# Kernel optimization log

Hardware: AMD Instinct MI355X
Metric: run time of the kernel (lower is better)

## Reference

```python
import jax, jax.numpy as jnp
import numpy as np

N, M = 1024, 32
FN, FE = 64, 32
AGG_N, AGG_E = 128, 64
OUT_N, OUT_E = 64, 32


def _build_indices(n, m):
    nip, eip = [], []
    k = 0
    for i in range(1, n):
        j0 = max(0, i - m)
        nip += list(range(j0, i))
        eip += list(range(k, k + i - j0))
        k += i - j0
    n1 = np.array(nip, np.int32)
    eT = np.array(eip, np.int32)
    n2 = np.concatenate([np.full(min(i, m), i, np.int32) for i in range(1, n)])
    # padded previous-node window indices (0 = zero pad slot)
    prev_nodes = np.zeros(n * m, np.int32)
    k = 0
    for i in range(n):
        t = min(i, m)
        prev_nodes[(i + 1) * m - t:(i + 1) * m] = np.arange(k, k + t) + 1
        k += t
    n_e = k
    norm_node = np.full(n, 1.0 / m, np.float32)
    for i in range(1, m):
        norm_node[i] = 1.0 / i
    prev_edges = np.zeros(n_e * m, np.int32)
    k = 0
    e = 0
    for i in range(n):
        j0 = max(0, i - m)
        for j in range(j0, i):
            if j > j0:
                prev_edges[(e + 1) * m - (j - j0):(e + 1) * m] = np.arange(k, k + j - j0) + 1
            e += 1
        k += i - j0
    norm_edge = np.ones(n_e, np.float32)
    k = 0
    for i in range(1, n):
        t = min(i, m)
        for j in range(t):
            if j > 0:
                norm_edge[k] = 1.0 / j
            k += 1
    return n1, eT, n2, prev_nodes, norm_node, prev_edges, norm_edge, n_e

N1, ET, N2, PREV_N, NORM_N, PREV_E, NORM_E, NE = _build_indices(N, M)
N1 = jnp.asarray(N1); ET = jnp.asarray(ET); N2 = jnp.asarray(N2)
PREV_N = jnp.asarray(PREV_N); PREV_E = jnp.asarray(PREV_E)
NORM_N = jnp.asarray(NORM_N); NORM_E = jnp.asarray(NORM_E)


def setup_inputs() -> dict:
    key = jax.random.key(0)
    ks = jax.random.split(key, 20)
    s = 0.02
    inp = {
        'input_nodes': jax.random.normal(ks[0], (2, N, FN), jnp.float32),
        'input_edges': jax.random.normal(ks[1], (2, NE, FE), jnp.float32),
        # node-branch MLPs (exclude_last=False)
        'Wan1': jax.random.normal(ks[2], (2 * FN + FE, 2 * AGG_N)) * s,
        'ban1': jnp.zeros((2 * AGG_N,)),
        'Wan2': jax.random.normal(ks[3], (2 * AGG_N, AGG_N)) * s,
        'ban2': jnp.zeros((AGG_N,)),
        'Wln1': jax.random.normal(ks[4], (AGG_N + FN, AGG_N + FN)) * s,
        'bln1': jnp.zeros((AGG_N + FN,)),
        'Wln2': jax.random.normal(ks[5], (AGG_N + FN, OUT_N)) * s,
        'bln2': jnp.zeros((OUT_N,)),
        # edge-branch MLPs
        'Wae1': jax.random.normal(ks[6], (FN + FE, 2 * AGG_E)) * s,
        'bae1': jnp.zeros((2 * AGG_E,)),
        'Wae2': jax.random.normal(ks[7], (2 * AGG_E, AGG_E)) * s,
        'bae2': jnp.zeros((AGG_E,)),
        'Wle1': jax.random.normal(ks[8], (AGG_E + FE, AGG_E + FE)) * s,
        'ble1': jnp.zeros((AGG_E + FE,)),
        'Wle2': jax.random.normal(ks[9], (AGG_E + FE, OUT_E)) * s,
        'ble2': jnp.zeros((OUT_E,)),
    }
    return inp


def _mlp2(x, W1, b1, W2, b2):
    return jax.nn.relu(jax.nn.relu(x @ W1 + b1) @ W2 + b2)


def reference(input_nodes, input_edges, Wan1, ban1, Wan2, ban2, Wln1, bln1, Wln2, bln2,
              Wae1, bae1, Wae2, bae2, Wle1, ble1, Wle2, ble2):
    B = input_nodes.shape[0]
    # gather node-edge pairs [B, NE, FN+FE] and node-edge-node triples [B, NE, 2FN+FE]
    pairs = jnp.concatenate([input_nodes[:, N1], input_edges[:, ET]], axis=-1)
    triples = jnp.concatenate([input_nodes[:, N1], input_edges[:, ET], input_nodes[:, N2]], axis=-1)
    # node branch (exclude_last=False -> triples)
    hn = _mlp2(triples, Wan1, ban1, Wan2, ban2)                     # [B, NE, AGG_N]
    hn = jnp.concatenate([jnp.zeros((B, 1, AGG_N), hn.dtype), hn], axis=1)
    pn = hn[:, PREV_N].reshape(B, N, M, AGG_N).sum(axis=2)          # padded window sum
    pn = pn * NORM_N[None, :, None]
    nodes_in = jnp.concatenate([pn, input_nodes], axis=-1)
    out_nodes = _mlp2(nodes_in, Wln1, bln1, Wln2, bln2)             # activation_nodes = relu
    # edge branch (pairs)
    he = _mlp2(pairs, Wae1, bae1, Wae2, bae2)                       # [B, NE, AGG_E]
    he = jnp.concatenate([jnp.zeros((B, 1, AGG_E), he.dtype), he], axis=1)
    pe = he[:, PREV_E].reshape(B, NE, M, AGG_E).sum(axis=2)
    pe = pe * NORM_E[None, :, None]
    edges_in = jnp.concatenate([pe, input_edges], axis=-1)
    out_edges = _mlp2(edges_in, Wle1, ble1, Wle2, ble2)             # activation_edges = relu
    return out_nodes, out_edges
```

## Files before the change

kernel.cpp:

```cpp
#include <hip/hip_runtime.h>
#include <cstdint>

#define NN    1024
#define MM    32
#define NEDGE 32240
#define MROWS 64480
#define PX    168
#define PST   392
#define PLB   104
#define PHE   72

typedef unsigned short ushort_t;

typedef __bf16 bf16x8 __attribute__((ext_vector_type(8)));
typedef float  floatx4 __attribute__((ext_vector_type(4)));

__device__ __forceinline__ float b2f(ushort_t u) {
    union { unsigned int i; float f; } v; v.i = ((unsigned int)u) << 16; return v.f;
}
__device__ __forceinline__ ushort_t f2b(float f) {
    return __builtin_bit_cast(ushort_t, (__bf16)f);
}
__device__ __forceinline__ int edge_base(int i) {
    return (i <= MM) ? ((i * (i - 1)) >> 1) : (496 + (i - MM) * MM);
}

__global__ __launch_bounds__(256) void k_pack(
        const float* an1, const float* an2, const float* ae1, const float* ae2,
        const float* le1, const float* le2, const float* ln1, const float* ln2,
        const float* nodes,
        ushort_t* pan1, ushort_t* pan2, ushort_t* pae1, ushort_t* pae2,
        ushort_t* ple1, ushort_t* ple2, ushort_t* pln1, ushort_t* pln2,
        ushort_t* nodesb) {
    __shared__ float tile[32][33];
    const int bid = blockIdx.x;
    const int tid = threadIdx.x;
    if (bid < 152) {
        const float* s; ushort_t* d; int K, N, t;
        if (bid < 40)       { s = an1; d = pan1; K = 160; N = 256; t = bid;       }
        else if (bid < 72)  { s = an2; d = pan2; K = 256; N = 128; t = bid - 40;  }
        else if (bid < 84)  { s = ae1; d = pae1; K = 96;  N = 128; t = bid - 72;  }
        else if (bid < 92)  { s = ae2; d = pae2; K = 128; N = 64;  t = bid - 84;  }
        else if (bid < 101) { s = le1; d = ple1; K = 96;  N = 96;  t = bid - 92;  }
        else if (bid < 104) { s = le2; d = ple2; K = 96;  N = 32;  t = bid - 101; }
        else if (bid < 140) { s = ln1; d = pln1; K = 192; N = 192; t = bid - 104; }
        else                { s = ln2; d = pln2; K = 192; N = 64;  t = bid - 140; }
        int ntn = N >> 5;
        int tk = t / ntn, tn = t - tk * ntn;
        int k0 = tk * 32, n0 = tn * 32;
        int tx = tid & 31, ty = tid >> 5;
#pragma unroll
        for (int m = 0; m < 4; ++m)
            tile[ty + m * 8][tx] = s[(size_t)(k0 + ty + m * 8) * N + n0 + tx];
        __syncthreads();
#pragma unroll
        for (int m = 0; m < 4; ++m)
            d[(size_t)(n0 + ty + m * 8) * K + k0 + tx] = f2b(tile[tx][ty + m * 8]);
    } else {
        int i4 = (bid - 152) * 256 + tid;
        float4 v = ((const float4*)nodes)[i4];
        uint2 o;
        o.x = (unsigned)f2b(v.x) | ((unsigned)f2b(v.y) << 16);
        o.y = (unsigned)f2b(v.z) | ((unsigned)f2b(v.w) << 16);
        ((uint2*)nodesb)[i4] = o;
    }
}

__global__ __launch_bounds__(512, 4) void k_main(
        const ushort_t* __restrict__ nodesb, const float* __restrict__ edges,
        const ushort_t* __restrict__ pan1, const float* __restrict__ ban1,
        const ushort_t* __restrict__ pan2, const float* __restrict__ ban2,
        const ushort_t* __restrict__ pae1, const float* __restrict__ bae1,
        const ushort_t* __restrict__ pae2, const float* __restrict__ bae2,
        const ushort_t* __restrict__ ple1, const float* __restrict__ ble1,
        const ushort_t* __restrict__ ple2, const float* __restrict__ ble2,
        ushort_t* __restrict__ pn, float* __restrict__ out_edges) {
    __shared__ alignas(16) ushort_t X[32 * PX];
    __shared__ alignas(16) ushort_t H[32 * PST];
    __shared__ alignas(16) ushort_t HE[32 * PHE];
    const int tid = threadIdx.x;
    const int w = tid >> 6, l = tid & 63, lrow = l & 15, lq = l >> 4;
    const int bid = blockIdx.x;
    floatx4 zero = {0.f, 0.f, 0.f, 0.f};

    const int b = bid >> 10, i = bid & 1023;
    const int t = min(i, MM);
    if (i == 0) {
        if (tid < 64) ((unsigned*)(pn + (size_t)bid * 128))[tid] = 0u;
        return;
    }
    const int j0 = i - t;
    const int base = b * NEDGE + edge_base(i);

    bf16x8 B0[5], B1[5], B2[3];
#pragma unroll
    for (int kt = 0; kt < 5; ++kt) {
        B0[kt] = *(const bf16x8*)(pan1 + (size_t)(16 * w + lrow) * 160 + kt * 32 + lq * 8);
        B1[kt] = *(const bf16x8*)(pan1 + (size_t)(16 * (w + 8) + lrow) * 160 + kt * 32 + lq * 8);
    }
#pragma unroll
    for (int kt = 0; kt < 3; ++kt)
        B2[kt] = *(const bf16x8*)(pae1 + (size_t)(16 * w + lrow) * 96 + kt * 32 + lq * 8);
    const float c0 = ban1[16 * w + lrow];
    const float c1 = ban1[16 * (w + 8) + lrow];
    const float c2 = bae1[16 * w + lrow];

#pragma unroll
    for (int k = 0; k < 4; ++k) {
        int rr = w * 4 + k;
        unsigned* xr = (unsigned*)(X + rr * PX);
        const unsigned* nj = (const unsigned*)(nodesb + (size_t)(b * NN + j0 + rr) * 64);
        const unsigned* ni = (const unsigned*)(nodesb + (size_t)(b * NN + i) * 64);
        if (l < 32) { xr[l] = nj[l]; xr[48 + l] = ni[l]; }
        else if (l < 48) {
            float2 e = *(const float2*)(edges + (size_t)(base + rr) * 32 + 2 * (l - 32));
            xr[l] = (unsigned)f2b(e.x) | ((unsigned)f2b(e.y) << 16);
        }
    }
    __syncthreads();

#pragma unroll
    for (int s = 0; s < 2; ++s) {
        bf16x8 A[5];
#pragma unroll
        for (int kt = 0; kt < 5; ++kt)
            A[kt] = *(const bf16x8*)&X[(s * 16 + lrow) * PX + kt * 32 + lq * 8];
        floatx4 a0 = zero, a1 = zero, a2 = zero;
#pragma unroll
        for (int kt = 0; kt < 5; ++kt) {
            a0 = __builtin_amdgcn_mfma_f32_16x16x32_bf16(A[kt], B0[kt], a0, 0, 0, 0);
            a1 = __builtin_amdgcn_mfma_f32_16x16x32_bf16(A[kt], B1[kt], a1, 0, 0, 0);
        }
#pragma unroll
        for (int kt = 0; kt < 3; ++kt)
            a2 = __builtin_amdgcn_mfma_f32_16x16x32_bf16(A[kt], B2[kt], a2, 0, 0, 0);
#pragma unroll
        for (int r_ = 0; r_ < 4; ++r_) {
            int row = (s * 16 + lq * 4 + r_) * PST;
            H[row + 16 * w + lrow]       = f2b(fmaxf(a0[r_] + c0, 0.f));
            H[row + 128 + 16 * w + lrow] = f2b(fmaxf(a1[r_] + c1, 0.f));
            H[row + 256 + 16 * w + lrow] = f2b(fmaxf(a2[r_] + c2, 0.f));
        }
    }
    __syncthreads();

    if (w < 4) {
        bf16x8 D0[8], D1[8];
#pragma unroll
        for (int kt = 0; kt < 8; ++kt) {
            D0[kt] = *(const bf16x8*)(pan2 + (size_t)(16 * w + lrow) * 256 + kt * 32 + lq * 8);
            D1[kt] = *(const bf16x8*)(pan2 + (size_t)(16 * (w + 4) + lrow) * 256 + kt * 32 + lq * 8);
        }
        float d0 = ban2[16 * w + lrow];
        float d1 = ban2[16 * (w + 4) + lrow];
        float P0 = 0.f, P1 = 0.f;
#pragma unroll
        for (int s = 0; s < 2; ++s) {
            floatx4 a0 = zero, a1 = zero;
#pragma unroll
            for (int kt = 0; kt < 8; ++kt) {
                bf16x8 a = *(const bf16x8*)&H[(s * 16 + lrow) * PST + kt * 32 + lq * 8];
                a0 = __builtin_amdgcn_mfma_f32_16x16x32_bf16(a, D0[kt], a0, 0, 0, 0);
                a1 = __builtin_amdgcn_mfma_f32_16x16x32_bf16(a, D1[kt], a1, 0, 0, 0);
            }
#pragma unroll
            for (int r_ = 0; r_ < 4; ++r_) {
                int row = s * 16 + lq * 4 + r_;
                float v0 = b2f(f2b(fmaxf(a0[r_] + d0, 0.f)));
                float v1 = b2f(f2b(fmaxf(a1[r_] + d1, 0.f)));
                if (row < t) { P0 += v0; P1 += v1; }
            }
        }
        P0 += __shfl_xor(P0, 16); P0 += __shfl_xor(P0, 32);
        P1 += __shfl_xor(P1, 16); P1 += __shfl_xor(P1, 32);
        if (l < 16) {
            float inv = 1.0f / (float)t;
            pn[(size_t)bid * 128 + 16 * w + lrow]       = f2b(P0 * inv);
            pn[(size_t)bid * 128 + 16 * (w + 4) + lrow] = f2b(P1 * inv);
        }
    } else {
        int u = w - 4;
        bf16x8 E[4];
#pragma unroll
        for (int kt = 0; kt < 4; ++kt)
            E[kt] = *(const bf16x8*)(pae2 + (size_t)(16 * u + lrow) * 128 + kt * 32 + lq * 8);
        float d2 = bae2[16 * u + lrow];
#pragma unroll
        for (int s = 0; s < 2; ++s) {
            floatx4 a2 = zero;
#pragma unroll
            for (int kt = 0; kt < 4; ++kt) {
                bf16x8 a = *(const bf16x8*)&H[(s * 16 + lrow) * PST + 256 + kt * 32 + lq * 8];
                a2 = __builtin_amdgcn_mfma_f32_16x16x32_bf16(a, E[kt], a2, 0, 0, 0);
            }
#pragma unroll
            for (int r_ = 0; r_ < 4; ++r_)
                HE[(s * 16 + lq * 4 + r_) * PHE + 16 * u + lrow] = f2b(fmaxf(a2[r_] + d2, 0.f));
        }
        if (l < 16) {
            float h[32];
#pragma unroll
            for (int p = 0; p < 32; ++p)
                h[p] = b2f(HE[p * PHE + 16 * u + l]);
            float run = 0.f;
#pragma unroll
            for (int p = 0; p < 32; ++p) {
                if (p < t)
                    X[p * PX + 16 * u + l] = f2b((p == 0) ? 0.f : run * (1.0f / (float)p));
                run += h[p];
            }
        }
    }
    __syncthreads();

    if (w < 6) {
        bf16x8 F0[3];
#pragma unroll
        for (int kt = 0; kt < 3; ++kt)
            F0[kt] = *(const bf16x8*)(ple1 + (size_t)(16 * w + lrow) * 96 + kt * 32 + lq * 8);
        float v0 = ble1[16 * w + lrow];
#pragma unroll
        for (int s = 0; s < 2; ++s) {
            bf16x8 A[3];
#pragma unroll
            for (int kt = 0; kt < 3; ++kt)
                A[kt] = *(const bf16x8*)&X[(s * 16 + lrow) * PX + kt * 32 + lq * 8];
            floatx4 a0 = zero;
#pragma unroll
            for (int kt = 0; kt < 3; ++kt)
                a0 = __builtin_amdgcn_mfma_f32_16x16x32_bf16(A[kt], F0[kt], a0, 0, 0, 0);
#pragma unroll
            for (int r_ = 0; r_ < 4; ++r_)
                H[(s * 16 + lq * 4 + r_) * PLB + 16 * w + lrow] = f2b(fmaxf(a0[r_] + v0, 0.f));
        }
    }
    __syncthreads();

    if (w < 4) {
        int ct = w & 1, s2 = w >> 1;
        int c0o = 16 * ct;
        bf16x8 F2[3];
#pragma unroll
        for (int kt = 0; kt < 3; ++kt)
            F2[kt] = *(const bf16x8*)(ple2 + (size_t)(c0o + lrow) * 96 + kt * 32 + lq * 8);
        float v2 = ble2[c0o + lrow];
        floatx4 a2 = zero;
#pragma unroll
        for (int kt = 0; kt < 3; ++kt) {
            bf16x8 a = *(const bf16x8*)&H[(s2 * 16 + lrow) * PLB + kt * 32 + lq * 8];
            a2 = __builtin_amdgcn_mfma_f32_16x16x32_bf16(a, F2[kt], a2, 0, 0, 0);
        }
#pragma unroll
        for (int r_ = 0; r_ < 4; ++r_) {
            int grow = s2 * 16 + lq * 4 + r_;
            if (grow < t)
                out_edges[(size_t)(base + grow) * 32 + c0o + lrow] = fmaxf(a2[r_] + v2, 0.f);
        }
    }
}

__global__ __launch_bounds__(192) void k_final(
        const ushort_t* __restrict__ pn, const ushort_t* __restrict__ nodesb,
        const ushort_t* __restrict__ pln1, const float* __restrict__ bln1,
        const ushort_t* __restrict__ pln2, const float* __restrict__ bln2,
        float* __restrict__ out_nodes) {
    __shared__ alignas(16) ushort_t LA[32 * 200];
    __shared__ alignas(16) ushort_t LB[32 * 200];
    const int tid = threadIdx.x;
    const int w = tid >> 6, l = tid & 63, lrow = l & 15, lq = l >> 4;
    floatx4 zero = {0.f, 0.f, 0.f, 0.f};

    int tile = blockIdx.x;
    for (int u = tid; u < 768; u += 192) {
        int row = u / 24, c = u - row * 24;
        int r = tile * 32 + row;
        const uint4* src = (c < 16) ? ((const uint4*)(pn + (size_t)r * 128) + c)
                                    : ((const uint4*)(nodesb + (size_t)r * 64) + (c - 16));
        *(uint4*)&LA[row * 200 + c * 8] = *src;
    }
    bf16x8 f1[6][4]; float v1[4];
#pragma unroll
    for (int kt = 0; kt < 6; ++kt)
#pragma unroll
        for (int nt = 0; nt < 4; ++nt)
            f1[kt][nt] = *(const bf16x8*)(pln1 + (size_t)(w * 64 + nt * 16 + lrow) * 192 + kt * 32 + lq * 8);
#pragma unroll
    for (int nt = 0; nt < 4; ++nt) v1[nt] = bln1[w * 64 + nt * 16 + lrow];
    __syncthreads();

    floatx4 acc[2][4];
#pragma unroll
    for (int s = 0; s < 2; ++s)
#pragma unroll
        for (int nt = 0; nt < 4; ++nt) acc[s][nt] = zero;
#pragma unroll
    for (int s = 0; s < 2; ++s)
#pragma unroll
        for (int kt = 0; kt < 6; ++kt) {
            bf16x8 a = *(const bf16x8*)&LA[(s * 16 + lrow) * 200 + kt * 32 + lq * 8];
#pragma unroll
            for (int nt = 0; nt < 4; ++nt)
                acc[s][nt] = __builtin_amdgcn_mfma_f32_16x16x32_bf16(a, f1[kt][nt], acc[s][nt], 0, 0, 0);
        }
#pragma unroll
    for (int s = 0; s < 2; ++s)
#pragma unroll
        for (int nt = 0; nt < 4; ++nt) {
            int col = w * 64 + nt * 16 + lrow;
#pragma unroll
            for (int r_ = 0; r_ < 4; ++r_)
                LB[(s * 16 + lq * 4 + r_) * 200 + col] = f2b(fmaxf(acc[s][nt][r_] + v1[nt], 0.f));
        }
    bf16x8 f2[6][2]; float v2[2] = {0.f, 0.f};
    if (w < 2) {
#pragma unroll
        for (int kt = 0; kt < 6; ++kt)
#pragma unroll
            for (int nt = 0; nt < 2; ++nt)
                f2[kt][nt] = *(const bf16x8*)(pln2 + (size_t)(w * 32 + nt * 16 + lrow) * 192 + kt * 32 + lq * 8);
#pragma unroll
        for (int nt = 0; nt < 2; ++nt) v2[nt] = bln2[w * 32 + nt * 16 + lrow];
    }
    __syncthreads();
    if (w < 2) {
        floatx4 a2[2][2];
#pragma unroll
        for (int s = 0; s < 2; ++s) { a2[s][0] = zero; a2[s][1] = zero; }
#pragma unroll
        for (int s = 0; s < 2; ++s)
#pragma unroll
            for (int kt = 0; kt < 6; ++kt) {
                bf16x8 a = *(const bf16x8*)&LB[(s * 16 + lrow) * 200 + kt * 32 + lq * 8];
#pragma unroll
                for (int nt = 0; nt < 2; ++nt)
                    a2[s][nt] = __builtin_amdgcn_mfma_f32_16x16x32_bf16(a, f2[kt][nt], a2[s][nt], 0, 0, 0);
            }
#pragma unroll
        for (int s = 0; s < 2; ++s)
#pragma unroll
            for (int nt = 0; nt < 2; ++nt) {
                int col = w * 32 + nt * 16 + lrow;
#pragma unroll
                for (int r_ = 0; r_ < 4; ++r_)
                    out_nodes[(size_t)(tile * 32 + s * 16 + lq * 4 + r_) * 64 + col] =
                        fmaxf(a2[s][nt][r_] + v2[nt], 0.f);
            }
    }
}

extern "C" void kernel_launch(void* const* d_in, const int* in_sizes, int n_in,
                              void* d_out, int out_size, void* d_ws, size_t ws_size,
                              hipStream_t stream) {
    const float* nodes = (const float*)d_in[0];
    const float* edges = (const float*)d_in[1];
    const float* Wan1 = (const float*)d_in[2];  const float* ban1 = (const float*)d_in[3];
    const float* Wan2 = (const float*)d_in[4];  const float* ban2 = (const float*)d_in[5];
    const float* Wln1 = (const float*)d_in[6];  const float* bln1 = (const float*)d_in[7];
    const float* Wln2 = (const float*)d_in[8];  const float* bln2 = (const float*)d_in[9];
    const float* Wae1 = (const float*)d_in[10]; const float* bae1 = (const float*)d_in[11];
    const float* Wae2 = (const float*)d_in[12]; const float* bae2 = (const float*)d_in[13];
    const float* Wle1 = (const float*)d_in[14]; const float* ble1 = (const float*)d_in[15];
    const float* Wle2 = (const float*)d_in[16]; const float* ble2 = (const float*)d_in[17];

    char* ws = (char*)d_ws;
    size_t o = 0;
    auto alloc = [&](size_t bytes) -> void* {
        void* r = ws + o;
        o += (bytes + 255) & ~(size_t)255;
        return r;
    };
    ushort_t* pn     = (ushort_t*)alloc((size_t)2048 * 128 * 2);
    ushort_t* nodesb = (ushort_t*)alloc((size_t)2 * NN * 64 * 2);
    ushort_t* pan1 = (ushort_t*)alloc(160 * 256 * 2);
    ushort_t* pan2 = (ushort_t*)alloc(256 * 128 * 2);
    ushort_t* pae1 = (ushort_t*)alloc(96 * 128 * 2);
    ushort_t* pae2 = (ushort_t*)alloc(128 * 64 * 2);
    ushort_t* ple1 = (ushort_t*)alloc(96 * 96 * 2);
    ushort_t* ple2 = (ushort_t*)alloc(96 * 32 * 2);
    ushort_t* pln1 = (ushort_t*)alloc(192 * 192 * 2);
    ushort_t* pln2 = (ushort_t*)alloc(192 * 64 * 2);

    float* out_nodes = (float*)d_out;
    float* out_edges = (float*)d_out + 2 * NN * 64;

    k_pack<<<280, 256, 0, stream>>>(Wan1, Wan2, Wae1, Wae2, Wle1, Wle2, Wln1, Wln2,
                                    nodes,
                                    pan1, pan2, pae1, pae2, ple1, ple2, pln1, pln2,
                                    nodesb);
    k_main<<<2048, 512, 0, stream>>>(nodesb, edges,
                                     pan1, ban1, pan2, ban2,
                                     pae1, bae1, pae2, bae2,
                                     ple1, ble1, ple2, ble2,
                                     pn, out_edges);
    k_final<<<64, 192, 0, stream>>>(pn, nodesb, pln1, bln1, pln2, bln2, out_nodes);

    (void)in_sizes; (void)n_in; (void)out_size; (void)ws_size;
}
```

Baseline: 154.9 us.

## Process both batch elements per block to reuse staged weights

Each k_main block now handles one node index for both batch elements, so the grid is halved and the per-wave weight fragments loaded into registers serve two batches. Per-stage weight and bias loads are hoisted ahead of the barriers so they overlap with the preceding stage. The shared-memory buffers are doubled to hold both batches, which raises LDS use per block and may reduce the number of blocks that fit on a CU. With only 1024 blocks there is also less parallelism available to hide latency.

```diff
diff --git a/kernel.cpp b/kernel.cpp
--- a/kernel.cpp
+++ b/kernel.cpp
@@ -75,22 +75,22 @@
         const ushort_t* __restrict__ ple1, const float* __restrict__ ble1,
         const ushort_t* __restrict__ ple2, const float* __restrict__ ble2,
         ushort_t* __restrict__ pn, float* __restrict__ out_edges) {
-    __shared__ alignas(16) ushort_t X[32 * PX];
-    __shared__ alignas(16) ushort_t H[32 * PST];
-    __shared__ alignas(16) ushort_t HE[32 * PHE];
+    __shared__ alignas(16) ushort_t X[2][32 * PX];
+    __shared__ alignas(16) ushort_t H[2][32 * PST];
+    __shared__ alignas(16) ushort_t HE[2][32 * PHE];
     const int tid = threadIdx.x;
     const int w = tid >> 6, l = tid & 63, lrow = l & 15, lq = l >> 4;
-    const int bid = blockIdx.x;
+    const int i = blockIdx.x;
+    const int t = min(i, MM);
     floatx4 zero = {0.f, 0.f, 0.f, 0.f};
 
-    const int b = bid >> 10, i = bid & 1023;
-    const int t = min(i, MM);
     if (i == 0) {
-        if (tid < 64) ((unsigned*)(pn + (size_t)bid * 128))[tid] = 0u;
+        if (tid < 64)       ((unsigned*)pn)[tid] = 0u;
+        else if (tid < 128) ((unsigned*)(pn + (size_t)1024 * 128))[tid - 64] = 0u;
         return;
     }
     const int j0 = i - t;
-    const int base = b * NEDGE + edge_base(i);
+    const int eb0 = edge_base(i);
 
     bf16x8 B0[5], B1[5], B2[3];
 #pragma unroll
@@ -106,155 +106,183 @@
     const float c2 = bae1[16 * w + lrow];
 
 #pragma unroll
-    for (int k = 0; k < 4; ++k) {
-        int rr = w * 4 + k;
-        unsigned* xr = (unsigned*)(X + rr * PX);
-        const unsigned* nj = (const unsigned*)(nodesb + (size_t)(b * NN + j0 + rr) * 64);
-        const unsigned* ni = (const unsigned*)(nodesb + (size_t)(b * NN + i) * 64);
-        if (l < 32) { xr[l] = nj[l]; xr[48 + l] = ni[l]; }
-        else if (l < 48) {
-            float2 e = *(const float2*)(edges + (size_t)(base + rr) * 32 + 2 * (l - 32));
-            xr[l] = (unsigned)f2b(e.x) | ((unsigned)f2b(e.y) << 16);
-        }
-    }
-    __syncthreads();
-
-#pragma unroll
-    for (int s = 0; s < 2; ++s) {
-        bf16x8 A[5];
-#pragma unroll
-        for (int kt = 0; kt < 5; ++kt)
-            A[kt] = *(const bf16x8*)&X[(s * 16 + lrow) * PX + kt * 32 + lq * 8];
-        floatx4 a0 = zero, a1 = zero, a2 = zero;
-#pragma unroll
-        for (int kt = 0; kt < 5; ++kt) {
-            a0 = __builtin_amdgcn_mfma_f32_16x16x32_bf16(A[kt], B0[kt], a0, 0, 0, 0);
-            a1 = __builtin_amdgcn_mfma_f32_16x16x32_bf16(A[kt], B1[kt], a1, 0, 0, 0);
-        }
-#pragma unroll
-        for (int kt = 0; kt < 3; ++kt)
-            a2 = __builtin_amdgcn_mfma_f32_16x16x32_bf16(A[kt], B2[kt], a2, 0, 0, 0);
-#pragma unroll
-        for (int r_ = 0; r_ < 4; ++r_) {
-            int row = (s * 16 + lq * 4 + r_) * PST;
-            H[row + 16 * w + lrow]       = f2b(fmaxf(a0[r_] + c0, 0.f));
-            H[row + 128 + 16 * w + lrow] = f2b(fmaxf(a1[r_] + c1, 0.f));
-            H[row + 256 + 16 * w + lrow] = f2b(fmaxf(a2[r_] + c2, 0.f));
-        }
-    }
-    __syncthreads();
-
+    for (int bb = 0; bb < 2; ++bb) {
+        const int base = bb * NEDGE + eb0;
+#pragma unroll
+        for (int k = 0; k < 4; ++k) {
+            int rr = w * 4 + k;
+            unsigned* xr = (unsigned*)(X[bb] + rr * PX);
+            const unsigned* nj = (const unsigned*)(nodesb + (size_t)(bb * NN + j0 + rr) * 64);
+            const unsigned* ni = (const unsigned*)(nodesb + (size_t)(bb * NN + i) * 64);
+            if (l < 32) { xr[l] = nj[l]; xr[48 + l] = ni[l]; }
+            else if (l < 48) {
+                float2 e = *(const float2*)(edges + (size_t)(base + rr) * 32 + 2 * (l - 32));
+                xr[l] = (unsigned)f2b(e.x) | ((unsigned)f2b(e.y) << 16);
+            }
+        }
+    }
+    __syncthreads();
+
+#pragma unroll
+    for (int bb = 0; bb < 2; ++bb)
+#pragma unroll
+        for (int s = 0; s < 2; ++s) {
+            bf16x8 A[5];
+#pragma unroll
+            for (int kt = 0; kt < 5; ++kt)
+                A[kt] = *(const bf16x8*)&X[bb][(s * 16 + lrow) * PX + kt * 32 + lq * 8];
+            floatx4 a0 = zero, a1 = zero, a2 = zero;
+#pragma unroll
+            for (int kt = 0; kt < 5; ++kt) {
+                a0 = __builtin_amdgcn_mfma_f32_16x16x32_bf16(A[kt], B0[kt], a0, 0, 0, 0);
+                a1 = __builtin_amdgcn_mfma_f32_16x16x32_bf16(A[kt], B1[kt], a1, 0, 0, 0);
+            }
+#pragma unroll
+            for (int kt = 0; kt < 3; ++kt)
+                a2 = __builtin_amdgcn_mfma_f32_16x16x32_bf16(A[kt], B2[kt], a2, 0, 0, 0);
+#pragma unroll
+            for (int r_ = 0; r_ < 4; ++r_) {
+                int row = (s * 16 + lq * 4 + r_) * PST;
+                H[bb][row + 16 * w + lrow]       = f2b(fmaxf(a0[r_] + c0, 0.f));
+                H[bb][row + 128 + 16 * w + lrow] = f2b(fmaxf(a1[r_] + c1, 0.f));
+                H[bb][row + 256 + 16 * w + lrow] = f2b(fmaxf(a2[r_] + c2, 0.f));
+            }
+        }
+
+    bf16x8 D0[8], D1[8], E[4];
+    float d0 = 0.f, d1 = 0.f, d2 = 0.f;
     if (w < 4) {
-        bf16x8 D0[8], D1[8];
 #pragma unroll
         for (int kt = 0; kt < 8; ++kt) {
             D0[kt] = *(const bf16x8*)(pan2 + (size_t)(16 * w + lrow) * 256 + kt * 32 + lq * 8);
             D1[kt] = *(const bf16x8*)(pan2 + (size_t)(16 * (w + 4) + lrow) * 256 + kt * 32 + lq * 8);
         }
-        float d0 = ban2[16 * w + lrow];
-        float d1 = ban2[16 * (w + 4) + lrow];
-        float P0 = 0.f, P1 = 0.f;
-#pragma unroll
-        for (int s = 0; s < 2; ++s) {
-            floatx4 a0 = zero, a1 = zero;
-#pragma unroll
-            for (int kt = 0; kt < 8; ++kt) {
-                bf16x8 a = *(const bf16x8*)&H[(s * 16 + lrow) * PST + kt * 32 + lq * 8];
-                a0 = __builtin_amdgcn_mfma_f32_16x16x32_bf16(a, D0[kt], a0, 0, 0, 0);
-                a1 = __builtin_amdgcn_mfma_f32_16x16x32_bf16(a, D1[kt], a1, 0, 0, 0);
-            }
-#pragma unroll
-            for (int r_ = 0; r_ < 4; ++r_) {
-                int row = s * 16 + lq * 4 + r_;
-                float v0 = b2f(f2b(fmaxf(a0[r_] + d0, 0.f)));
-                float v1 = b2f(f2b(fmaxf(a1[r_] + d1, 0.f)));
-                if (row < t) { P0 += v0; P1 += v1; }
-            }
-        }
-        P0 += __shfl_xor(P0, 16); P0 += __shfl_xor(P0, 32);
-        P1 += __shfl_xor(P1, 16); P1 += __shfl_xor(P1, 32);
-        if (l < 16) {
-            float inv = 1.0f / (float)t;
-            pn[(size_t)bid * 128 + 16 * w + lrow]       = f2b(P0 * inv);
-            pn[(size_t)bid * 128 + 16 * (w + 4) + lrow] = f2b(P1 * inv);
-        }
+        d0 = ban2[16 * w + lrow];
+        d1 = ban2[16 * (w + 4) + lrow];
     } else {
         int u = w - 4;
-        bf16x8 E[4];
 #pragma unroll
         for (int kt = 0; kt < 4; ++kt)
             E[kt] = *(const bf16x8*)(pae2 + (size_t)(16 * u + lrow) * 128 + kt * 32 + lq * 8);
-        float d2 = bae2[16 * u + lrow];
-#pragma unroll
-        for (int s = 0; s < 2; ++s) {
-            floatx4 a2 = zero;
-#pragma unroll
-            for (int kt = 0; kt < 4; ++kt) {
-                bf16x8 a = *(const bf16x8*)&H[(s * 16 + lrow) * PST + 256 + kt * 32 + lq * 8];
-                a2 = __builtin_amdgcn_mfma_f32_16x16x32_bf16(a, E[kt], a2, 0, 0, 0);
-            }
-#pragma unroll
-            for (int r_ = 0; r_ < 4; ++r_)
-                HE[(s * 16 + lq * 4 + r_) * PHE + 16 * u + lrow] = f2b(fmaxf(a2[r_] + d2, 0.f));
-        }
+        d2 = bae2[16 * u + lrow];
+    }
+    __syncthreads();
+
+    if (w < 4) {
+#pragma unroll
+        for (int bb = 0; bb < 2; ++bb) {
+            float P0 = 0.f, P1 = 0.f;
+#pragma unroll
+            for (int s = 0; s < 2; ++s) {
+                floatx4 a0 = zero, a1 = zero;
+#pragma unroll
+                for (int kt = 0; kt < 8; ++kt) {
+                    bf16x8 a = *(const bf16x8*)&H[bb][(s * 16 + lrow) * PST + kt * 32 + lq * 8];
+                    a0 = __builtin_amdgcn_mfma_f32_16x16x32_bf16(a, D0[kt], a0, 0, 0, 0);
+                    a1 = __builtin_amdgcn_mfma_f32_16x16x32_bf16(a, D1[kt], a1, 0, 0, 0);
+                }
+#pragma unroll
+                for (int r_ = 0; r_ < 4; ++r_) {
+                    int row = s * 16 + lq * 4 + r_;
+                    float v0 = b2f(f2b(fmaxf(a0[r_] + d0, 0.f)));
+                    float v1 = b2f(f2b(fmaxf(a1[r_] + d1, 0.f)));
+                    if (row < t) { P0 += v0; P1 += v1; }
+                }
+            }
+            P0 += __shfl_xor(P0, 16); P0 += __shfl_xor(P0, 32);
+            P1 += __shfl_xor(P1, 16); P1 += __shfl_xor(P1, 32);
+            if (l < 16) {
+                float inv = 1.0f / (float)t;
+                pn[(size_t)(bb * 1024 + i) * 128 + 16 * w + lrow]       = f2b(P0 * inv);
+                pn[(size_t)(bb * 1024 + i) * 128 + 16 * (w + 4) + lrow] = f2b(P1 * inv);
+            }
+        }
+    } else {
+        int u = w - 4;
+#pragma unroll
+        for (int bb = 0; bb < 2; ++bb)
+#pragma unroll
+            for (int s = 0; s < 2; ++s) {
+                floatx4 a2 = zero;
+#pragma unroll
+                for (int kt = 0; kt < 4; ++kt) {
+                    bf16x8 a = *(const bf16x8*)&H[bb][(s * 16 + lrow) * PST + 256 + kt * 32 + lq * 8];
+                    a2 = __builtin_amdgcn_mfma_f32_16x16x32_bf16(a, E[kt], a2, 0, 0, 0);
+                }
+#pragma unroll
+                for (int r_ = 0; r_ < 4; ++r_)
+                    HE[bb][(s * 16 + lq * 4 + r_) * PHE + 16 * u + lrow] = f2b(fmaxf(a2[r_] + d2, 0.f));
+            }
         if (l < 16) {
-            float h[32];
-#pragma unroll
-            for (int p = 0; p < 32; ++p)
-                h[p] = b2f(HE[p * PHE + 16 * u + l]);
-            float run = 0.f;
-#pragma unroll
-            for (int p = 0; p < 32; ++p) {
-                if (p < t)
-                    X[p * PX + 16 * u + l] = f2b((p == 0) ? 0.f : run * (1.0f / (float)p));
-                run += h[p];
-            }
-        }
-    }
-    __syncthreads();
-
+#pragma unroll
+            for (int bb = 0; bb < 2; ++bb) {
+                float h[32];
+#pragma unroll
+                for (int p = 0; p < 32; ++p)
+                    h[p] = b2f(HE[bb][p * PHE + 16 * u + l]);
+                float run = 0.f;
+#pragma unroll
+                for (int p = 0; p < 32; ++p) {
+                    if (p < t)
+                        X[bb][p * PX + 16 * u + l] = f2b((p == 0) ? 0.f : run * (1.0f / (float)p));
+                    run += h[p];
+                }
+            }
+        }
+    }
+    bf16x8 F0[3]; float v0 = 0.f;
     if (w < 6) {
-        bf16x8 F0[3];
 #pragma unroll
         for (int kt = 0; kt < 3; ++kt)
             F0[kt] = *(const bf16x8*)(ple1 + (size_t)(16 * w + lrow) * 96 + kt * 32 + lq * 8);
-        float v0 = ble1[16 * w + lrow];
-#pragma unroll
-        for (int s = 0; s < 2; ++s) {
-            bf16x8 A[3];
-#pragma unroll
-            for (int kt = 0; kt < 3; ++kt)
-                A[kt] = *(const bf16x8*)&X[(s * 16 + lrow) * PX + kt * 32 + lq * 8];
-            floatx4 a0 = zero;
-#pragma unroll
-            for (int kt = 0; kt < 3; ++kt)
-                a0 = __builtin_amdgcn_mfma_f32_16x16x32_bf16(A[kt], F0[kt], a0, 0, 0, 0);
-#pragma unroll
-            for (int r_ = 0; r_ < 4; ++r_)
-                H[(s * 16 + lq * 4 + r_) * PLB + 16 * w + lrow] = f2b(fmaxf(a0[r_] + v0, 0.f));
-        }
-    }
-    __syncthreads();
-
+        v0 = ble1[16 * w + lrow];
+    }
+    __syncthreads();
+
+    if (w < 6) {
+#pragma unroll
+        for (int bb = 0; bb < 2; ++bb)
+#pragma unroll
+            for (int s = 0; s < 2; ++s) {
+                bf16x8 A[3];
+#pragma unroll
+                for (int kt = 0; kt < 3; ++kt)
+                    A[kt] = *(const bf16x8*)&X[bb][(s * 16 + lrow) * PX + kt * 32 + lq * 8];
+                floatx4 a0 = zero;
+#pragma unroll
+                for (int kt = 0; kt < 3; ++kt)
+                    a0 = __builtin_amdgcn_mfma_f32_16x16x32_bf16(A[kt], F0[kt], a0, 0, 0, 0);
+#pragma unroll
+                for (int r_ = 0; r_ < 4; ++r_)
+                    H[bb][(s * 16 + lq * 4 + r_) * PLB + 16 * w + lrow] = f2b(fmaxf(a0[r_] + v0, 0.f));
+            }
+    }
+    const int ct = w & 1, s2 = w >> 1, c0o = 16 * ct;
+    bf16x8 F2[3]; float v2 = 0.f;
     if (w < 4) {
-        int ct = w & 1, s2 = w >> 1;
-        int c0o = 16 * ct;
-        bf16x8 F2[3];
 #pragma unroll
         for (int kt = 0; kt < 3; ++kt)
             F2[kt] = *(const bf16x8*)(ple2 + (size_t)(c0o + lrow) * 96 + kt * 32 + lq * 8);
-        float v2 = ble2[c0o + lrow];
-        floatx4 a2 = zero;
-#pragma unroll
-        for (int kt = 0; kt < 3; ++kt) {
-            bf16x8 a = *(const bf16x8*)&H[(s2 * 16 + lrow) * PLB + kt * 32 + lq * 8];
-            a2 = __builtin_amdgcn_mfma_f32_16x16x32_bf16(a, F2[kt], a2, 0, 0, 0);
-        }
-#pragma unroll
-        for (int r_ = 0; r_ < 4; ++r_) {
-            int grow = s2 * 16 + lq * 4 + r_;
-            if (grow < t)
-                out_edges[(size_t)(base + grow) * 32 + c0o + lrow] = fmaxf(a2[r_] + v2, 0.f);
+        v2 = ble2[c0o + lrow];
+    }
+    __syncthreads();
+
+    if (w < 4) {
+#pragma unroll
+        for (int bb = 0; bb < 2; ++bb) {
+            floatx4 a2 = zero;
+#pragma unroll
+            for (int kt = 0; kt < 3; ++kt) {
+                bf16x8 a = *(const bf16x8*)&H[bb][(s2 * 16 + lrow) * PLB + kt * 32 + lq * 8];
+                a2 = __builtin_amdgcn_mfma_f32_16x16x32_bf16(a, F2[kt], a2, 0, 0, 0);
+            }
+            const int base = bb * NEDGE + eb0;
+#pragma unroll
+            for (int r_ = 0; r_ < 4; ++r_) {
+                int grow = s2 * 16 + lq * 4 + r_;
+                if (grow < t)
+                    out_edges[(size_t)(base + grow) * 32 + c0o + lrow] = fmaxf(a2[r_] + v2, 0.f);
+            }
         }
     }
 }
@@ -387,7 +415,7 @@
                                     nodes,
                                     pan1, pan2, pae1, pae2, ple1, ple2, pln1, pln2,
                                     nodesb);
-    k_main<<<2048, 512, 0, stream>>>(nodesb, edges,
+    k_main<<<1024, 512, 0, stream>>>(nodesb, edges,
                                      pan1, ban1, pan2, ban2,
                                      pae1, bae1, pae2, bae2,
                                      ple1, ble1, ple2, ble2,
```

After: 141.4 us (median of 2 runs). 8.7% less time.
